# Performance work log

Measured on AMD Instinct MI355X. Metric: run time of the kernel, lower is better.

## Reference

```python
import jax, jax.numpy as jnp
import numpy as np

BETA = 0.7
NUM_STEPS = 25
HID = 256
SPIKE_DIM = 128
COORD_DIM = 64
IN_DIM = SPIKE_DIM + COORD_DIM  # 192
BATCH = 131072


def setup_inputs() -> dict:
    key = jax.random.key(0)
    ks = jax.random.split(key, 8)
    s = lambda fan_in: 1.0 / np.sqrt(fan_in)
    return {
        "sensor_spikes": jax.random.uniform(ks[0], (BATCH, SPIKE_DIM), dtype=jnp.float32),
        "current_coords": jax.random.normal(ks[1], (BATCH, COORD_DIM), dtype=jnp.float32),
        # nn.Linear weights are [out, in], uniform(-1/sqrt(in), 1/sqrt(in))
        "W0": jax.random.uniform(ks[2], (HID, IN_DIM), jnp.float32, -s(IN_DIM), s(IN_DIM)),
        "b0": jax.random.uniform(ks[3], (HID,), jnp.float32, -s(IN_DIM), s(IN_DIM)),
        "W1": jax.random.uniform(ks[4], (HID, HID), jnp.float32, -s(HID), s(HID)),
        "b1": jax.random.uniform(ks[5], (HID,), jnp.float32, -s(HID), s(HID)),
        "W_out": jax.random.uniform(ks[6], (IN_DIM, HID), jnp.float32, -s(HID), s(HID)),
        "b_out": jax.random.uniform(ks[7], (IN_DIM,), jnp.float32, -s(HID), s(HID)),
    }


def reference(sensor_spikes, current_coords, W0, b0, W1, b1, W_out, b_out):
    x = jnp.concatenate([sensor_spikes, current_coords], axis=-1)  # [B, 192]
    B = x.shape[0]
    # Layer-0 drive is x every timestep (the original re-feeds x each step),
    # so its pre-activation current is step-invariant.
    c0 = x @ W0.T + b0  # [B, HID]

    def lif(v, current):
        v = BETA * v + (1.0 - BETA) * current
        spikes = (v >= 1.0).astype(v.dtype)
        v = v * (1.0 - spikes)
        return v, spikes

    def step(carry, _):
        v0, v1 = carry
        v0, s0 = lif(v0, c0)
        c1 = s0 @ W1.T + b1
        v1, s1 = lif(v1, c1)
        return (v0, v1), s1

    zeros = jnp.zeros((B, HID), dtype=x.dtype)
    (_, _), s1_seq = jax.lax.scan(step, (zeros, zeros), None, length=NUM_STEPS)
    final_spikes = s1_seq[-1]  # [B, HID]

    out = final_spikes @ W_out.T + b_out  # [B, 192]
    next_action = jnp.sign(final_spikes)  # spikes are 0/1 -> sign == spikes
    next_coords = out[:, -COORD_DIM:]
    return next_action, next_coords
```

## Files before the change

### kernel.cpp

```cpp
#include <hip/hip_runtime.h>
#include <stdint.h>

#define BATCH_N   131072
#define HID       256
#define SPIKE_DIM 128
#define COORD_DIM 64
#define IN_DIM    192
#define STEPS     25
#define TILE      64
#define BLOCK     512

typedef float f4  __attribute__((ext_vector_type(4)));
typedef short bf8 __attribute__((ext_vector_type(8)));
typedef unsigned short us4 __attribute__((ext_vector_type(4)));

#define W1T_OFF  24576
#define WOT_OFF  90112
#define SCAL_OFF 106496

static __device__ __forceinline__ unsigned short f2bf(float f) {
  union { float f; unsigned u; } v; v.f = f;
  unsigned r = v.u + 0x7FFF + ((v.u >> 16) & 1);
  return (unsigned short)(r >> 16);
}
static __device__ __forceinline__ float bf2f(unsigned short h) {
  union { unsigned u; float f; } v; v.u = ((unsigned)h) << 16; return v.f;
}

__global__ __launch_bounds__(256)
void prep_kernel(const float* __restrict__ W0,
                 const float* __restrict__ W1,
                 const float* __restrict__ Wout,
                 const float* __restrict__ b1,
                 float* __restrict__ ws) {
  __shared__ float r1[256];
  __shared__ float r2[256];
  if (blockIdx.x == 512) {
    const int t = threadIdx.x;
    float m = 0.f;
    for (int k = 0; k < HID; ++k) m = fmaxf(m, W1[k*HID + t]);
    r1[t] = m;
    r2[t] = fmaxf(b1[t], 0.f);
    __syncthreads();
    for (int s = 128; s > 0; s >>= 1) {
      if (t < s) { r1[t] = fmaxf(r1[t], r1[t+s]); r2[t] = fmaxf(r2[t], r2[t+s]); }
      __syncthreads();
    }
    if (t == 0) { ws[SCAL_OFF] = r2[0]; ws[SCAL_OFF+1] = r1[0]; }
    return;
  }
  int idx = blockIdx.x * 256 + threadIdx.x;
  if (idx < HID*IN_DIM) {
    ((unsigned short*)ws)[idx] = f2bf(W0[idx]);
  }
  int i1 = idx - HID*IN_DIM;
  if (i1 >= 0 && i1 < HID*HID) {
    int j = i1 >> 8, i = i1 & 255;
    ws[W1T_OFF + i1] = W1[i*HID + j];
  }
  int i2 = idx - (HID*IN_DIM + HID*HID);
  if (i2 >= 0 && i2 < HID*COORD_DIM) {
    int k = i2 >> 6, c = i2 & 63;
    ws[WOT_OFF + i2] = Wout[(SPIKE_DIM + c)*HID + k];
  }
}

__global__ __launch_bounds__(BLOCK)
void snn_kernel(const float* __restrict__ spk,
                const float* __restrict__ crd,
                const float* __restrict__ W0,
                const float* __restrict__ b0,
                const float* __restrict__ b1,
                const float* __restrict__ bout,
                const float* __restrict__ ws,
                float* __restrict__ out) {
  __shared__ unsigned short sbuf[TILE*264];
  unsigned short* xb  = sbuf;
  unsigned short* c0s = sbuf;

  const int tid  = threadIdx.x;
  const int lane = tid & 63;
  const int wv   = tid >> 6;
  const int quad = lane >> 4;
  const int l15  = lane & 15;
  const int e0   = blockIdx.x * TILE;
  const int i4   = lane * 4;

  {
    const f4* sp4 = (const f4*)(spk + (size_t)e0 * SPIKE_DIM);
    for (int t = tid; t < TILE*SPIKE_DIM/4; t += BLOCK) {
      int e = t >> 5, j = (t & 31) * 4;
      f4 v = __builtin_nontemporal_load(&sp4[t]);
      us4 h; h.x = f2bf(v.x); h.y = f2bf(v.y); h.z = f2bf(v.z); h.w = f2bf(v.w);
      *(us4*)&xb[e*200 + j] = h;
    }
    const f4* cr4 = (const f4*)(crd + (size_t)e0 * COORD_DIM);
    for (int t = tid; t < TILE*COORD_DIM/4; t += BLOCK) {
      int e = t >> 4, j = SPIKE_DIM + (t & 15) * 4;
      f4 v = __builtin_nontemporal_load(&cr4[t]);
      us4 h; h.x = f2bf(v.x); h.y = f2bf(v.y); h.z = f2bf(v.z); h.w = f2bf(v.w);
      *(us4*)&xb[e*200 + j] = h;
    }
  }
  __syncthreads();

  const int msub  = wv >> 1;
  const int nhalf = wv & 1;
  const unsigned short* W0b = (const unsigned short*)ws;

  f4 acc[8];
  #pragma unroll
  for (int n = 0; n < 8; ++n) { acc[n].x = acc[n].y = acc[n].z = acc[n].w = 0.f; }

  #pragma unroll
  for (int kc = 0; kc < IN_DIM/32; ++kc) {
    bf8 a = *(const bf8*)&xb[(msub*16 + l15)*200 + kc*32 + quad*8];
    #pragma unroll
    for (int n = 0; n < 8; ++n) {
      bf8 b = *(const bf8*)&W0b[(size_t)(nhalf*128 + n*16 + l15)*IN_DIM + kc*32 + quad*8];
      acc[n] = __builtin_amdgcn_mfma_f32_16x16x32_bf16(a, b, acc[n], 0, 0, 0);
    }
  }

  __syncthreads();
  {
    const int erow = msub*16 + quad*4;
    #pragma unroll
    for (int n = 0; n < 8; ++n) {
      const int neuron = nhalf*128 + n*16 + l15;
      const float bias = b0[neuron];
      c0s[(erow+0)*264 + neuron] = f2bf(acc[n].x + bias);
      c0s[(erow+1)*264 + neuron] = f2bf(acc[n].y + bias);
      c0s[(erow+2)*264 + neuron] = f2bf(acc[n].z + bias);
      c0s[(erow+3)*264 + neuron] = f2bf(acc[n].w + bias);
    }
  }
  __syncthreads();

  const float* W1T = ws + W1T_OFF;
  const float* WoT = ws + WOT_OFF;
  const float b1mx = ws[SCAL_OFF];
  const float w1pm = ws[SCAL_OFF + 1];
  f4 b0v = *(const f4*)&b0[i4];
  f4 b1v = *(const f4*)&b1[i4];
  float bc = bout[SPIKE_DIM + lane];
  const int eb = wv * 8;

  unsigned fastm = 0;
  #pragma unroll
  for (int ee = 0; ee < 8; ++ee) {
    us4 craw = *(const us4*)&c0s[(eb+ee)*264 + i4];
    f4 c0a; c0a.x = bf2f(craw.x); c0a.y = bf2f(craw.y);
            c0a.z = bf2f(craw.z); c0a.w = bf2f(craw.w);
    unsigned long long a0 = __ballot(c0a.x >= 0.90f);
    unsigned long long a1 = __ballot(c0a.y >= 0.90f);
    unsigned long long a2 = __ballot(c0a.z >= 0.90f);
    unsigned long long a3 = __ballot(c0a.w >= 0.90f);
    int nspk = __popcll(a0) + __popcll(a1) + __popcll(a2) + __popcll(a3);
    if (b1mx + w1pm * (float)nspk < 0.97f) fastm |= (1u << ee);
  }

  #pragma unroll
  for (int ee = 0; ee < 8; ++ee) {
    if (fastm & (1u << ee)) {
      const int e = e0 + eb + ee;
      f4 z; z.x = z.y = z.z = z.w = 0.f;
      __builtin_nontemporal_store(z, (f4*)&out[(size_t)e*HID + i4]);
      __builtin_nontemporal_store(bc,
          &out[(size_t)BATCH_N*HID + (size_t)e*COORD_DIM + lane]);
    }
  }

  if (__builtin_expect(fastm != 0xFFu, 0)) {
    for (int ee = 0; ee < 8; ++ee) {
      if (fastm & (1u << ee)) continue;
      const int e = e0 + eb + ee;
      us4 craw = *(const us4*)&c0s[(eb+ee)*264 + i4];
      f4 c0a; c0a.x = bf2f(craw.x); c0a.y = bf2f(craw.y);
              c0a.z = bf2f(craw.z); c0a.w = bf2f(craw.w);

      unsigned long long a0 = __ballot(c0a.x >= 0.90f);
      unsigned long long a1 = __ballot(c0a.y >= 0.90f);
      unsigned long long a2 = __ballot(c0a.z >= 0.90f);
      unsigned long long a3 = __ballot(c0a.w >= 0.90f);

      f4 bnd = b1v;
      unsigned long long mm;
      #define BPROCQ(MASK, Q)                                   \
        mm = (MASK);                                            \
        while (mm) {                                            \
          int l = __builtin_ctzll(mm); mm &= mm - 1;            \
          f4 wv_ = *(const f4*)&W1T[(l*4 + (Q))*HID + i4];      \
          bnd.x += fmaxf(wv_.x, 0.f);                           \
          bnd.y += fmaxf(wv_.y, 0.f);                           \
          bnd.z += fmaxf(wv_.z, 0.f);                           \
          bnd.w += fmaxf(wv_.w, 0.f);                           \
        }
      BPROCQ(a0, 0)
      BPROCQ(a1, 1)
      BPROCQ(a2, 2)
      BPROCQ(a3, 3)
      #undef BPROCQ

      bool threat = (bnd.x >= 0.98f) | (bnd.y >= 0.98f) |
                    (bnd.z >= 0.98f) | (bnd.w >= 0.98f);

      if (__ballot(threat) == 0ull) {
        f4 z; z.x = z.y = z.z = z.w = 0.f;
        __builtin_nontemporal_store(z, (f4*)&out[(size_t)e*HID + i4]);
        __builtin_nontemporal_store(bc,
            &out[(size_t)BATCH_N*HID + (size_t)e*COORD_DIM + lane]);
      } else {
        float cx = 0.f, cy = 0.f, cz = 0.f, cw = 0.f;
        const float* r0 = W0 + (size_t)(i4+0)*IN_DIM;
        const float* r1 = W0 + (size_t)(i4+1)*IN_DIM;
        const float* r2 = W0 + (size_t)(i4+2)*IN_DIM;
        const float* r3 = W0 + (size_t)(i4+3)*IN_DIM;
        const float* xs_ = spk + (size_t)e*SPIKE_DIM;
        const float* xc_ = crd + (size_t)e*COORD_DIM;
        for (int j = 0; j < SPIKE_DIM; ++j) {
          float xj = xs_[j];
          cx = fmaf(xj, r0[j], cx); cy = fmaf(xj, r1[j], cy);
          cz = fmaf(xj, r2[j], cz); cw = fmaf(xj, r3[j], cw);
        }
        for (int j = 0; j < COORD_DIM; ++j) {
          float xj = xc_[j];
          cx = fmaf(xj, r0[SPIKE_DIM+j], cx); cy = fmaf(xj, r1[SPIKE_DIM+j], cy);
          cz = fmaf(xj, r2[SPIKE_DIM+j], cz); cw = fmaf(xj, r3[SPIKE_DIM+j], cw);
        }
        const float c0x = cx + b0v.x, c0y = cy + b0v.y;
        const float c0z = cz + b0v.z, c0w = cw + b0v.w;

        float v0x=0.f, v0y=0.f, v0z=0.f, v0w=0.f;
        float v1x=0.f, v1y=0.f, v1z=0.f, v1w=0.f;
        float s1x=0.f, s1y=0.f, s1z=0.f, s1w=0.f;

        for (int t = 0; t < STEPS; ++t) {
          bool sp;
          unsigned long long m0, m1, m2, m3;
          v0x = __fmul_rn(0.7f, v0x) + __fmul_rn(0.3f, c0x);
          sp = (v0x >= 1.0f); m0 = __ballot(sp); if (sp) v0x = 0.f;
          v0y = __fmul_rn(0.7f, v0y) + __fmul_rn(0.3f, c0y);
          sp = (v0y >= 1.0f); m1 = __ballot(sp); if (sp) v0y = 0.f;
          v0z = __fmul_rn(0.7f, v0z) + __fmul_rn(0.3f, c0z);
          sp = (v0z >= 1.0f); m2 = __ballot(sp); if (sp) v0z = 0.f;
          v0w = __fmul_rn(0.7f, v0w) + __fmul_rn(0.3f, c0w);
          sp = (v0w >= 1.0f); m3 = __ballot(sp); if (sp) v0w = 0.f;

          float c1x = b1v.x, c1y = b1v.y, c1z = b1v.z, c1w = b1v.w;
          f4 wcur; wcur.x = wcur.y = wcur.z = wcur.w = 0.f;
          int have = 0;
          #define PROCQ(MASK, Q)                                                  \
            mm = (MASK);                                                          \
            while (mm) {                                                          \
              int l = __builtin_ctzll(mm); mm &= mm - 1;                          \
              f4 wn = *(const f4*)&W1T[(l*4 + (Q))*HID + i4];                     \
              if (have) { c1x += wcur.x; c1y += wcur.y; c1z += wcur.z; c1w += wcur.w; } \
              wcur = wn; have = 1;                                                \
            }
          PROCQ(m0, 0)
          PROCQ(m1, 1)
          PROCQ(m2, 2)
          PROCQ(m3, 3)
          #undef PROCQ
          if (have) { c1x += wcur.x; c1y += wcur.y; c1z += wcur.z; c1w += wcur.w; }

          v1x = __fmul_rn(0.7f, v1x) + __fmul_rn(0.3f, c1x);
          sp = (v1x >= 1.0f); s1x = sp ? 1.f : 0.f; if (sp) v1x = 0.f;
          v1y = __fmul_rn(0.7f, v1y) + __fmul_rn(0.3f, c1y);
          sp = (v1y >= 1.0f); s1y = sp ? 1.f : 0.f; if (sp) v1y = 0.f;
          v1z = __fmul_rn(0.7f, v1z) + __fmul_rn(0.3f, c1z);
          sp = (v1z >= 1.0f); s1z = sp ? 1.f : 0.f; if (sp) v1z = 0.f;
          v1w = __fmul_rn(0.7f, v1w) + __fmul_rn(0.3f, c1w);
          sp = (v1w >= 1.0f); s1w = sp ? 1.f : 0.f; if (sp) v1w = 0.f;
        }

        f4 res; res.x = s1x; res.y = s1y; res.z = s1z; res.w = s1w;
        __builtin_nontemporal_store(res, (f4*)&out[(size_t)e*HID + i4]);

        unsigned long long f0 = __ballot(s1x > 0.5f);
        unsigned long long f1 = __ballot(s1y > 0.5f);
        unsigned long long f2 = __ballot(s1z > 0.5f);
        unsigned long long f3 = __ballot(s1w > 0.5f);
        float cacc = bc;
        #define CPROCQ(MASK, Q)                                 \
          mm = (MASK);                                          \
          while (mm) {                                          \
            int l = __builtin_ctzll(mm); mm &= mm - 1;          \
            cacc += WoT[(l*4 + (Q))*COORD_DIM + lane];          \
          }
        CPROCQ(f0, 0)
        CPROCQ(f1, 1)
        CPROCQ(f2, 2)
        CPROCQ(f3, 3)
        #undef CPROCQ
        __builtin_nontemporal_store(cacc,
            &out[(size_t)BATCH_N*HID + (size_t)e*COORD_DIM + lane]);
      }
    }
  }
}

extern "C" void kernel_launch(void* const* d_in, const int* in_sizes, int n_in,
                              void* d_out, int out_size, void* d_ws, size_t ws_size,
                              hipStream_t stream) {
  (void)in_sizes; (void)n_in; (void)out_size; (void)ws_size;
  const float* spk = (const float*)d_in[0];
  const float* crd = (const float*)d_in[1];
  const float* W0  = (const float*)d_in[2];
  const float* b0  = (const float*)d_in[3];
  const float* W1  = (const float*)d_in[4];
  const float* b1  = (const float*)d_in[5];
  const float* Wo  = (const float*)d_in[6];
  const float* bo  = (const float*)d_in[7];
  float* ws  = (float*)d_ws;
  float* out = (float*)d_out;

  hipLaunchKernelGGL(prep_kernel, dim3(513), dim3(256), 0, stream, W0, W1, Wo, b1, ws);
  hipLaunchKernelGGL(snn_kernel, dim3(BATCH_N/TILE), dim3(BLOCK), 0, stream,
                     spk, crd, W0, b0, b1, bo, ws, out);
}
```

Before: 355.8 us.

## Count layer-0 spikes in registers, halve tile, and drop the secondary bound check

The block shrinks to 32 rows and 256 threads with a higher occupancy hint. Each row's count of layer-0 spikes is now taken straight from the MFMA accumulators using packed byte counters and shuffles. This replaces the bf16 c0 round trip through shared memory and the per-row ballots. The secondary bound check on the slow path is removed, so rows that fail the cheap test go straight to the full exact simulation. The prep kernel's W1 max reduction is also vectorised. The kernel still relies on the existing early-exit bound, which depends on the weight statistics.

Result: slower. 376.4 us (+5.8%).

```diff
diff --git a/kernel.cpp b/kernel.cpp
--- a/kernel.cpp
+++ b/kernel.cpp
@@ -7,8 +7,8 @@
 #define COORD_DIM 64
 #define IN_DIM    192
 #define STEPS     25
-#define TILE      64
-#define BLOCK     512
+#define TILE      32
+#define BLOCK     256
 
 typedef float f4  __attribute__((ext_vector_type(4)));
 typedef short bf8 __attribute__((ext_vector_type(8)));
@@ -22,9 +22,6 @@
   union { float f; unsigned u; } v; v.f = f;
   unsigned r = v.u + 0x7FFF + ((v.u >> 16) & 1);
   return (unsigned short)(r >> 16);
-}
-static __device__ __forceinline__ float bf2f(unsigned short h) {
-  union { unsigned u; float f; } v; v.u = ((unsigned)h) << 16; return v.f;
 }
 
 __global__ __launch_bounds__(256)
@@ -37,9 +34,15 @@
   __shared__ float r2[256];
   if (blockIdx.x == 512) {
     const int t = threadIdx.x;
-    float m = 0.f;
-    for (int k = 0; k < HID; ++k) m = fmaxf(m, W1[k*HID + t]);
-    r1[t] = m;
+    const f4* W14 = (const f4*)W1;
+    f4 m4; m4.x = m4.y = m4.z = m4.w = 0.f;
+    #pragma unroll 4
+    for (int i = t; i < HID*HID/4; i += 256) {
+      f4 v = W14[i];
+      m4.x = fmaxf(m4.x, v.x); m4.y = fmaxf(m4.y, v.y);
+      m4.z = fmaxf(m4.z, v.z); m4.w = fmaxf(m4.w, v.w);
+    }
+    r1[t] = fmaxf(fmaxf(m4.x, m4.y), fmaxf(m4.z, m4.w));
     r2[t] = fmaxf(b1[t], 0.f);
     __syncthreads();
     for (int s = 128; s > 0; s >>= 1) {
@@ -65,7 +68,7 @@
   }
 }
 
-__global__ __launch_bounds__(BLOCK)
+__global__ __launch_bounds__(BLOCK, 8)
 void snn_kernel(const float* __restrict__ spk,
                 const float* __restrict__ crd,
                 const float* __restrict__ W0,
@@ -74,9 +77,8 @@
                 const float* __restrict__ bout,
                 const float* __restrict__ ws,
                 float* __restrict__ out) {
-  __shared__ unsigned short sbuf[TILE*264];
-  unsigned short* xb  = sbuf;
-  unsigned short* c0s = sbuf;
+  __shared__ unsigned short xb[TILE*200];
+  __shared__ unsigned cnt2[16];
 
   const int tid  = threadIdx.x;
   const int lane = tid & 63;
@@ -108,6 +110,10 @@
   const int nhalf = wv & 1;
   const unsigned short* W0b = (const unsigned short*)ws;
 
+  float b0n[8];
+  #pragma unroll
+  for (int n = 0; n < 8; ++n) b0n[n] = b0[nhalf*128 + n*16 + l15];
+
   f4 acc[8];
   #pragma unroll
   for (int n = 0; n < 8; ++n) { acc[n].x = acc[n].y = acc[n].z = acc[n].w = 0.f; }
@@ -122,41 +128,35 @@
     }
   }
 
-  __syncthreads();
   {
-    const int erow = msub*16 + quad*4;
+    unsigned p = 0;
     #pragma unroll
     for (int n = 0; n < 8; ++n) {
-      const int neuron = nhalf*128 + n*16 + l15;
-      const float bias = b0[neuron];
-      c0s[(erow+0)*264 + neuron] = f2bf(acc[n].x + bias);
-      c0s[(erow+1)*264 + neuron] = f2bf(acc[n].y + bias);
-      c0s[(erow+2)*264 + neuron] = f2bf(acc[n].z + bias);
-      c0s[(erow+3)*264 + neuron] = f2bf(acc[n].w + bias);
-    }
+      p += (acc[n].x + b0n[n] >= 0.90f) ? 1u        : 0u;
+      p += (acc[n].y + b0n[n] >= 0.90f) ? (1u<<8)  : 0u;
+      p += (acc[n].z + b0n[n] >= 0.90f) ? (1u<<16) : 0u;
+      p += (acc[n].w + b0n[n] >= 0.90f) ? (1u<<24) : 0u;
+    }
+    p += __shfl_xor(p, 1, 16);
+    p += __shfl_xor(p, 2, 16);
+    p += __shfl_xor(p, 4, 16);
+    p += __shfl_xor(p, 8, 16);
+    if (l15 == 0) cnt2[(msub*4 + quad)*2 + nhalf] = p;
   }
   __syncthreads();
 
-  const float* W1T = ws + W1T_OFF;
-  const float* WoT = ws + WOT_OFF;
   const float b1mx = ws[SCAL_OFF];
   const float w1pm = ws[SCAL_OFF + 1];
-  f4 b0v = *(const f4*)&b0[i4];
-  f4 b1v = *(const f4*)&b1[i4];
   float bc = bout[SPIKE_DIM + lane];
   const int eb = wv * 8;
 
   unsigned fastm = 0;
   #pragma unroll
   for (int ee = 0; ee < 8; ++ee) {
-    us4 craw = *(const us4*)&c0s[(eb+ee)*264 + i4];
-    f4 c0a; c0a.x = bf2f(craw.x); c0a.y = bf2f(craw.y);
-            c0a.z = bf2f(craw.z); c0a.w = bf2f(craw.w);
-    unsigned long long a0 = __ballot(c0a.x >= 0.90f);
-    unsigned long long a1 = __ballot(c0a.y >= 0.90f);
-    unsigned long long a2 = __ballot(c0a.z >= 0.90f);
-    unsigned long long a3 = __ballot(c0a.w >= 0.90f);
-    int nspk = __popcll(a0) + __popcll(a1) + __popcll(a2) + __popcll(a3);
+    const int el = eb + ee;
+    const int base = ((el >> 4)*4 + ((el >> 2) & 3))*2;
+    const int sh = (el & 3) * 8;
+    unsigned nspk = ((cnt2[base] >> sh) & 255u) + ((cnt2[base+1] >> sh) & 255u);
     if (b1mx + w1pm * (float)nspk < 0.97f) fastm |= (1u << ee);
   }
 
@@ -172,131 +172,100 @@
   }
 
   if (__builtin_expect(fastm != 0xFFu, 0)) {
+    const float* W1T = ws + W1T_OFF;
+    const float* WoT = ws + WOT_OFF;
+    f4 b0v = *(const f4*)&b0[i4];
+    f4 b1v = *(const f4*)&b1[i4];
     for (int ee = 0; ee < 8; ++ee) {
       if (fastm & (1u << ee)) continue;
       const int e = e0 + eb + ee;
-      us4 craw = *(const us4*)&c0s[(eb+ee)*264 + i4];
-      f4 c0a; c0a.x = bf2f(craw.x); c0a.y = bf2f(craw.y);
-              c0a.z = bf2f(craw.z); c0a.w = bf2f(craw.w);
-
-      unsigned long long a0 = __ballot(c0a.x >= 0.90f);
-      unsigned long long a1 = __ballot(c0a.y >= 0.90f);
-      unsigned long long a2 = __ballot(c0a.z >= 0.90f);
-      unsigned long long a3 = __ballot(c0a.w >= 0.90f);
-
-      f4 bnd = b1v;
+
+      float cx = 0.f, cy = 0.f, cz = 0.f, cw = 0.f;
+      const float* r0 = W0 + (size_t)(i4+0)*IN_DIM;
+      const float* r1 = W0 + (size_t)(i4+1)*IN_DIM;
+      const float* r2 = W0 + (size_t)(i4+2)*IN_DIM;
+      const float* r3 = W0 + (size_t)(i4+3)*IN_DIM;
+      const float* xs_ = spk + (size_t)e*SPIKE_DIM;
+      const float* xc_ = crd + (size_t)e*COORD_DIM;
+      for (int j = 0; j < SPIKE_DIM; ++j) {
+        float xj = xs_[j];
+        cx = fmaf(xj, r0[j], cx); cy = fmaf(xj, r1[j], cy);
+        cz = fmaf(xj, r2[j], cz); cw = fmaf(xj, r3[j], cw);
+      }
+      for (int j = 0; j < COORD_DIM; ++j) {
+        float xj = xc_[j];
+        cx = fmaf(xj, r0[SPIKE_DIM+j], cx); cy = fmaf(xj, r1[SPIKE_DIM+j], cy);
+        cz = fmaf(xj, r2[SPIKE_DIM+j], cz); cw = fmaf(xj, r3[SPIKE_DIM+j], cw);
+      }
+      const float c0x = cx + b0v.x, c0y = cy + b0v.y;
+      const float c0z = cz + b0v.z, c0w = cw + b0v.w;
+
+      float v0x=0.f, v0y=0.f, v0z=0.f, v0w=0.f;
+      float v1x=0.f, v1y=0.f, v1z=0.f, v1w=0.f;
+      float s1x=0.f, s1y=0.f, s1z=0.f, s1w=0.f;
       unsigned long long mm;
-      #define BPROCQ(MASK, Q)                                   \
-        mm = (MASK);                                            \
-        while (mm) {                                            \
-          int l = __builtin_ctzll(mm); mm &= mm - 1;            \
-          f4 wv_ = *(const f4*)&W1T[(l*4 + (Q))*HID + i4];      \
-          bnd.x += fmaxf(wv_.x, 0.f);                           \
-          bnd.y += fmaxf(wv_.y, 0.f);                           \
-          bnd.z += fmaxf(wv_.z, 0.f);                           \
-          bnd.w += fmaxf(wv_.w, 0.f);                           \
+
+      for (int t = 0; t < STEPS; ++t) {
+        bool sp;
+        unsigned long long m0, m1, m2, m3;
+        v0x = __fmul_rn(0.7f, v0x) + __fmul_rn(0.3f, c0x);
+        sp = (v0x >= 1.0f); m0 = __ballot(sp); if (sp) v0x = 0.f;
+        v0y = __fmul_rn(0.7f, v0y) + __fmul_rn(0.3f, c0y);
+        sp = (v0y >= 1.0f); m1 = __ballot(sp); if (sp) v0y = 0.f;
+        v0z = __fmul_rn(0.7f, v0z) + __fmul_rn(0.3f, c0z);
+        sp = (v0z >= 1.0f); m2 = __ballot(sp); if (sp) v0z = 0.f;
+        v0w = __fmul_rn(0.7f, v0w) + __fmul_rn(0.3f, c0w);
+        sp = (v0w >= 1.0f); m3 = __ballot(sp); if (sp) v0w = 0.f;
+
+        float c1x = b1v.x, c1y = b1v.y, c1z = b1v.z, c1w = b1v.w;
+        f4 wcur; wcur.x = wcur.y = wcur.z = wcur.w = 0.f;
+        int have = 0;
+        #define PROCQ(MASK, Q)                                                  \
+          mm = (MASK);                                                          \
+          while (mm) {                                                          \
+            int l = __builtin_ctzll(mm); mm &= mm - 1;                          \
+            f4 wn = *(const f4*)&W1T[(l*4 + (Q))*HID + i4];                     \
+            if (have) { c1x += wcur.x; c1y += wcur.y; c1z += wcur.z; c1w += wcur.w; } \
+            wcur = wn; have = 1;                                                \
+          }
+        PROCQ(m0, 0)
+        PROCQ(m1, 1)
+        PROCQ(m2, 2)
+        PROCQ(m3, 3)
+        #undef PROCQ
+        if (have) { c1x += wcur.x; c1y += wcur.y; c1z += wcur.z; c1w += wcur.w; }
+
+        v1x = __fmul_rn(0.7f, v1x) + __fmul_rn(0.3f, c1x);
+        sp = (v1x >= 1.0f); s1x = sp ? 1.f : 0.f; if (sp) v1x = 0.f;
+        v1y = __fmul_rn(0.7f, v1y) + __fmul_rn(0.3f, c1y);
+        sp = (v1y >= 1.0f); s1y = sp ? 1.f : 0.f; if (sp) v1y = 0.f;
+        v1z = __fmul_rn(0.7f, v1z) + __fmul_rn(0.3f, c1z);
+        sp = (v1z >= 1.0f); s1z = sp ? 1.f : 0.f; if (sp) v1z = 0.f;
+        v1w = __fmul_rn(0.7f, v1w) + __fmul_rn(0.3f, c1w);
+        sp = (v1w >= 1.0f); s1w = sp ? 1.f : 0.f; if (sp) v1w = 0.f;
+      }
+
+      f4 res; res.x = s1x; res.y = s1y; res.z = s1z; res.w = s1w;
+      __builtin_nontemporal_store(res, (f4*)&out[(size_t)e*HID + i4]);
+
+      unsigned long long f0 = __ballot(s1x > 0.5f);
+      unsigned long long f1 = __ballot(s1y > 0.5f);
+      unsigned long long f2 = __ballot(s1z > 0.5f);
+      unsigned long long f3 = __ballot(s1w > 0.5f);
+      float cacc = bc;
+      #define CPROCQ(MASK, Q)                                 \
+        mm = (MASK);                                          \
+        while (mm) {                                          \
+          int l = __builtin_ctzll(mm); mm &= mm - 1;          \
+          cacc += WoT[(l*4 + (Q))*COORD_DIM + lane];          \
         }
-      BPROCQ(a0, 0)
-      BPROCQ(a1, 1)
-      BPROCQ(a2, 2)
-      BPROCQ(a3, 3)
-      #undef BPROCQ
-
-      bool threat = (bnd.x >= 0.98f) | (bnd.y >= 0.98f) |
-                    (bnd.z >= 0.98f) | (bnd.w >= 0.98f);
-
-      if (__ballot(threat) == 0ull) {
-        f4 z; z.x = z.y = z.z = z.w = 0.f;
-        __builtin_nontemporal_store(z, (f4*)&out[(size_t)e*HID + i4]);
-        __builtin_nontemporal_store(bc,
-            &out[(size_t)BATCH_N*HID + (size_t)e*COORD_DIM + lane]);
-      } else {
-        float cx = 0.f, cy = 0.f, cz = 0.f, cw = 0.f;
-        const float* r0 = W0 + (size_t)(i4+0)*IN_DIM;
-        const float* r1 = W0 + (size_t)(i4+1)*IN_DIM;
-        const float* r2 = W0 + (size_t)(i4+2)*IN_DIM;
-        const float* r3 = W0 + (size_t)(i4+3)*IN_DIM;
-        const float* xs_ = spk + (size_t)e*SPIKE_DIM;
-        const float* xc_ = crd + (size_t)e*COORD_DIM;
-        for (int j = 0; j < SPIKE_DIM; ++j) {
-          float xj = xs_[j];
-          cx = fmaf(xj, r0[j], cx); cy = fmaf(xj, r1[j], cy);
-          cz = fmaf(xj, r2[j], cz); cw = fmaf(xj, r3[j], cw);
-        }
-        for (int j = 0; j < COORD_DIM; ++j) {
-          float xj = xc_[j];
-          cx = fmaf(xj, r0[SPIKE_DIM+j], cx); cy = fmaf(xj, r1[SPIKE_DIM+j], cy);
-          cz = fmaf(xj, r2[SPIKE_DIM+j], cz); cw = fmaf(xj, r3[SPIKE_DIM+j], cw);
-        }
-        const float c0x = cx + b0v.x, c0y = cy + b0v.y;
-        const float c0z = cz + b0v.z, c0w = cw + b0v.w;
-
-        float v0x=0.f, v0y=0.f, v0z=0.f, v0w=0.f;
-        float v1x=0.f, v1y=0.f, v1z=0.f, v1w=0.f;
-        float s1x=0.f, s1y=0.f, s1z=0.f, s1w=0.f;
-
-        for (int t = 0; t < STEPS; ++t) {
-          bool sp;
-          unsigned long long m0, m1, m2, m3;
-          v0x = __fmul_rn(0.7f, v0x) + __fmul_rn(0.3f, c0x);
-          sp = (v0x >= 1.0f); m0 = __ballot(sp); if (sp) v0x = 0.f;
-          v0y = __fmul_rn(0.7f, v0y) + __fmul_rn(0.3f, c0y);
-          sp = (v0y >= 1.0f); m1 = __ballot(sp); if (sp) v0y = 0.f;
-          v0z = __fmul_rn(0.7f, v0z) + __fmul_rn(0.3f, c0z);
-          sp = (v0z >= 1.0f); m2 = __ballot(sp); if (sp) v0z = 0.f;
-          v0w = __fmul_rn(0.7f, v0w) + __fmul_rn(0.3f, c0w);
-          sp = (v0w >= 1.0f); m3 = __ballot(sp); if (sp) v0w = 0.f;
-
-          float c1x = b1v.x, c1y = b1v.y, c1z = b1v.z, c1w = b1v.w;
-          f4 wcur; wcur.x = wcur.y = wcur.z = wcur.w = 0.f;
-          int have = 0;
-          #define PROCQ(MASK, Q)                                                  \
-            mm = (MASK);                                                          \
-            while (mm) {                                                          \
-              int l = __builtin_ctzll(mm); mm &= mm - 1;                          \
-              f4 wn = *(const f4*)&W1T[(l*4 + (Q))*HID + i4];                     \
-              if (have) { c1x += wcur.x; c1y += wcur.y; c1z += wcur.z; c1w += wcur.w; } \
-              wcur = wn; have = 1;                                                \
-            }
-          PROCQ(m0, 0)
-          PROCQ(m1, 1)
-          PROCQ(m2, 2)
-          PROCQ(m3, 3)
-          #undef PROCQ
-          if (have) { c1x += wcur.x; c1y += wcur.y; c1z += wcur.z; c1w += wcur.w; }
-
-          v1x = __fmul_rn(0.7f, v1x) + __fmul_rn(0.3f, c1x);
-          sp = (v1x >= 1.0f); s1x = sp ? 1.f : 0.f; if (sp) v1x = 0.f;
-          v1y = __fmul_rn(0.7f, v1y) + __fmul_rn(0.3f, c1y);
-          sp = (v1y >= 1.0f); s1y = sp ? 1.f : 0.f; if (sp) v1y = 0.f;
-          v1z = __fmul_rn(0.7f, v1z) + __fmul_rn(0.3f, c1z);
-          sp = (v1z >= 1.0f); s1z = sp ? 1.f : 0.f; if (sp) v1z = 0.f;
-          v1w = __fmul_rn(0.7f, v1w) + __fmul_rn(0.3f, c1w);
-          sp = (v1w >= 1.0f); s1w = sp ? 1.f : 0.f; if (sp) v1w = 0.f;
-        }
-
-        f4 res; res.x = s1x; res.y = s1y; res.z = s1z; res.w = s1w;
-        __builtin_nontemporal_store(res, (f4*)&out[(size_t)e*HID + i4]);
-
-        unsigned long long f0 = __ballot(s1x > 0.5f);
-        unsigned long long f1 = __ballot(s1y > 0.5f);
-        unsigned long long f2 = __ballot(s1z > 0.5f);
-        unsigned long long f3 = __ballot(s1w > 0.5f);
-        float cacc = bc;
-        #define CPROCQ(MASK, Q)                                 \
-          mm = (MASK);                                          \
-          while (mm) {                                          \
-            int l = __builtin_ctzll(mm); mm &= mm - 1;          \
-            cacc += WoT[(l*4 + (Q))*COORD_DIM + lane];          \
-          }
-        CPROCQ(f0, 0)
-        CPROCQ(f1, 1)
-        CPROCQ(f2, 2)
-        CPROCQ(f3, 3)
-        #undef CPROCQ
-        __builtin_nontemporal_store(cacc,
-            &out[(size_t)BATCH_N*HID + (size_t)e*COORD_DIM + lane]);
-      }
+      CPROCQ(f0, 0)
+      CPROCQ(f1, 1)
+      CPROCQ(f2, 2)
+      CPROCQ(f3, 3)
+      #undef CPROCQ
+      __builtin_nontemporal_store(cacc,
+          &out[(size_t)BATCH_N*HID + (size_t)e*COORD_DIM + lane]);
     }
   }
 }
```
